# Performance work log

Hardware: AMD Instinct MI355X
Metric: run time of the kernel (lower is better)

The kernel has to match this reference:

```python
import jax, jax.numpy as jnp
import numpy as np

# dims
B, N, D, F, L = 512, 128, 256, 16, 3
EPS = 1e-7
MAX_NORM = 1.0 - 1e-5  # PoincareBall proj boundary (c = 1.0)


def _proj(x):
    """Project points into the open Poincare ball (c=1)."""
    n = jnp.maximum(jnp.linalg.norm(x, axis=-1, keepdims=True), EPS)
    scale = jnp.where(n > MAX_NORM, MAX_NORM / n, 1.0)
    return x * scale


def _expmap0(u):
    """Exponential map at the origin, c=1: tanh(||u||) * u / ||u||."""
    n = jnp.maximum(jnp.linalg.norm(u, axis=-1, keepdims=True), EPS)
    return jnp.tanh(n) * u / n


def _logmap0(x):
    """Log map at the origin, c=1: artanh(||x||) * x / ||x||."""
    n = jnp.maximum(jnp.linalg.norm(x, axis=-1, keepdims=True), EPS)
    return jnp.arctanh(jnp.minimum(n, MAX_NORM)) * x / n


def setup_inputs() -> dict:
    key = jax.random.key(0)
    ks = jax.random.split(key, 6)
    # manifold input points: small tangent vectors -> inside the ball
    x = 0.01 * jax.random.normal(ks[0], (B, N, D), dtype=jnp.float32)
    adj = jax.random.uniform(ks[1], (B, N, N), dtype=jnp.float32)
    node_mask = jnp.ones((B, N, 1), dtype=jnp.float32)
    # per-layer HGC linear weights (tangent-space linear), hidden_dim -> hidden_dim
    Ws = jax.random.normal(ks[2], (L, D, D), dtype=jnp.float32) / np.sqrt(D)
    bs = jnp.zeros((L, D), dtype=jnp.float32)
    # final masked linear: hidden_dim -> max_feat_num
    Wout = jax.random.normal(ks[3], (D, F), dtype=jnp.float32) / np.sqrt(D)
    bout = jnp.zeros((F,), dtype=jnp.float32)
    return {"x": x, "adj": adj, "node_mask": node_mask,
            "Ws": Ws, "bs": bs, "Wout": Wout, "bout": bout}


def reference(x, adj, node_mask, Ws, bs, Wout, bout):
    # HGCN decoder: stack of hyperbolic graph-conv layers on the Poincare ball
    # (logmap0 -> tangent linear -> adjacency aggregation -> ReLU -> expmap0),
    # then logmap0 and a masked linear head.
    h = _proj(x)
    for i in range(L):
        t = _logmap0(h)                                  # [B,N,D] tangent at origin
        t = t @ Ws[i] + bs[i]                            # tangent linear
        t = jnp.einsum('bij,bjd->bid', adj, t)           # sum aggregation, norm factor 1
        t = jax.nn.relu(t)                               # activation in tangent space
        h = _proj(_expmap0(t))                           # back to the manifold
    out_tan = _logmap0(h)                                # manifold.logmap0 decode
    type_pred = (out_tan @ Wout + bout) * node_mask      # [B,N,F]
    return type_pred
```

## Files before the change

kernel.cpp:

```cpp
#include <hip/hip_runtime.h>
#include <hip/hip_bf16.h>
#include <math.h>


typedef _Float16 f16;
typedef f16 f16x8 __attribute__((ext_vector_type(8)));
typedef f16 f16x4 __attribute__((ext_vector_type(4)));
typedef float f32x4 __attribute__((ext_vector_type(4)));

#define NB 512
#define NN 128
#define ND 256
#define NF 16
#define NL 3

#define EPSV   1e-7f
#define MAXN   0.99999f
#define ATHMAX 6.1030340f

__device__ __forceinline__ int sT_idx(int m, int k) {
    return m * ND + ((((k >> 3) ^ (m & 7)) << 3) | (k & 7));
}
__device__ __forceinline__ int sV_idx(int n, int j) {
    return n * NN + ((((j >> 3) ^ (n & 15)) << 3) | (j & 7));
}

__global__ void prep_kernel(const float* __restrict__ Ws,
                            const float* __restrict__ Wout,
                            f16* __restrict__ Wt, f16* __restrict__ WoutT) {
    int idx = blockIdx.x * 256 + threadIdx.x;
    if (idx < NL * ND * ND) {
        int l = idx / (ND * ND);
        int r = idx % (ND * ND);
        int n = r >> 8;
        int k = r & 255;
        Wt[idx] = (f16)Ws[l * ND * ND + k * ND + n];
    }
    if (idx < NF * ND) {
        int f = idx >> 8;
        int k = idx & 255;
        WoutT[idx] = (f16)Wout[k * NF + f];
    }
}

__global__ __launch_bounds__(1024, 4)
void hgcn_kernel(const float* __restrict__ x,
                 const float* __restrict__ adj,
                 const float* __restrict__ node_mask,
                 const f16*  __restrict__ Wt,
                 const float* __restrict__ bs,
                 const f16*  __restrict__ WoutT,
                 const float* __restrict__ bout,
                 float* __restrict__ out) {
    __shared__ __align__(16) f16 sT[NN * ND];
    __shared__ __align__(16) f16 sV[ND * NN];
    __shared__ float sRed[16 * 16];

    const int b    = blockIdx.x;
    const int tid  = threadIdx.x;
    const int wave = tid >> 6;
    const int lane = tid & 63;
    const int lg   = lane >> 4;
    const int lc   = lane & 15;

    const f32x4 fzero = {0.f, 0.f, 0.f, 0.f};

    {
        const float4* xb = (const float4*)(x + (size_t)b * NN * ND);
        #pragma unroll
        for (int r = 0; r < 8; ++r) {
            int row = wave * 8 + r;
            float4 v = xb[row * 64 + lane];
            float ssq = v.x * v.x + v.y * v.y + v.z * v.z + v.w * v.w;
            #pragma unroll
            for (int d = 1; d < 64; d <<= 1) ssq += __shfl_xor(ssq, d);
            float norm = sqrtf(ssq);
            float n1  = fmaxf(norm, EPSV);
            float sc1 = (n1 > MAXN) ? (MAXN / n1) : 1.0f;
            float hn  = norm * sc1;
            float n2  = fmaxf(hn, EPSV);
            float aa  = fminf(n2, MAXN);
            float s   = sc1 * (atanhf(aa) / n2);
            f16x4 t4;
            t4[0] = (f16)(v.x * s); t4[1] = (f16)(v.y * s);
            t4[2] = (f16)(v.z * s); t4[3] = (f16)(v.w * s);
            *(f16x4*)&sT[sT_idx(row, lane * 4)] = t4;
        }
    }

    f16x8 adjf[4];
    {
        const float* adjb = adj + (size_t)b * NN * NN;
        #pragma unroll
        for (int ks = 0; ks < 4; ++ks) {
            const float4* ap = (const float4*)(adjb + ((wave >> 1) * 16 + lc) * NN + ks * 32 + lg * 8);
            float4 alo = ap[0], ahi = ap[1];
            f16x8 a;
            a[0] = (f16)alo.x; a[1] = (f16)alo.y; a[2] = (f16)alo.z; a[3] = (f16)alo.w;
            a[4] = (f16)ahi.x; a[5] = (f16)ahi.y; a[6] = (f16)ahi.z; a[7] = (f16)ahi.w;
            adjf[ks] = a;
        }
    }
    __syncthreads();

    for (int layer = 0; layer < NL; ++layer) {
        const f16* WtL  = Wt + layer * ND * ND;
        const float bias = bs[layer * ND + wave * 16 + lc];

        f32x4 acc_a[8];
        #pragma unroll
        for (int t = 0; t < 8; ++t) acc_a[t] = fzero;

        #pragma unroll
        for (int ks = 0; ks < 8; ++ks) {
            f16x8 bfr = *(const f16x8*)(WtL + (wave * 16 + lc) * ND + ks * 32 + lg * 8);
            #pragma unroll
            for (int mt = 0; mt < 8; ++mt) {
                f16x8 afr = *(const f16x8*)&sT[sT_idx(mt * 16 + lc, ks * 32 + lg * 8)];
                acc_a[mt] = __builtin_amdgcn_mfma_f32_16x16x32_f16(afr, bfr, acc_a[mt], 0, 0, 0);
            }
        }
        #pragma unroll
        for (int mt = 0; mt < 8; ++mt) {
            f16x4 v;
            #pragma unroll
            for (int r = 0; r < 4; ++r) v[r] = (f16)(acc_a[mt][r] + bias);
            *(f16x4*)&sV[sV_idx(wave * 16 + lc, mt * 16 + lg * 4)] = v;
        }
        __syncthreads();

        f32x4 acc_b[8];
        #pragma unroll
        for (int t = 0; t < 8; ++t) acc_b[t] = fzero;

        #pragma unroll
        for (int ks = 0; ks < 4; ++ks) {
            #pragma unroll
            for (int nt = 0; nt < 8; ++nt) {
                f16x8 afr = *(const f16x8*)&sV[sV_idx(((wave & 1) * 8 + nt) * 16 + lc, ks * 32 + lg * 8)];
                acc_b[nt] = __builtin_amdgcn_mfma_f32_16x16x32_f16(afr, adjf[ks], acc_b[nt], 0, 0, 0);
            }
        }

        float ssq = 0.f;
        #pragma unroll
        for (int t = 0; t < 8; ++t)
            #pragma unroll
            for (int r = 0; r < 4; ++r) {
                float v = fmaxf(acc_b[t][r], 0.0f);
                acc_b[t][r] = v;
                ssq += v * v;
            }
        ssq += __shfl_xor(ssq, 16);
        ssq += __shfl_xor(ssq, 32);
        if (lg == 0) sRed[wave * 16 + lc] = ssq;
        __syncthreads();
        float tot = ssq + sRed[(wave ^ 1) * 16 + lc];
        float nu = sqrtf(tot);
        float scale = (nu > ATHMAX) ? (ATHMAX / nu) : 1.0f;

        #pragma unroll
        for (int nt = 0; nt < 8; ++nt) {
            f16x4 v;
            #pragma unroll
            for (int r = 0; r < 4; ++r) v[r] = (f16)(acc_b[nt][r] * scale);
            *(f16x4*)&sT[sT_idx((wave >> 1) * 16 + lc, ((wave & 1) * 8 + nt) * 16 + lg * 4)] = v;
        }
        __syncthreads();
    }

    if (wave < 8) {
        f32x4 acc = fzero;
        #pragma unroll
        for (int ks = 0; ks < 8; ++ks) {
            f16x8 afr = *(const f16x8*)&sT[sT_idx(wave * 16 + lc, ks * 32 + lg * 8)];
            f16x8 bfr = *(const f16x8*)(WoutT + lc * ND + ks * 32 + lg * 8);
            acc = __builtin_amdgcn_mfma_f32_16x16x32_f16(afr, bfr, acc, 0, 0, 0);
        }
        #pragma unroll
        for (int r = 0; r < 4; ++r) {
            int row = wave * 16 + lg * 4 + r;
            float mask = node_mask[b * NN + row];
            out[((size_t)b * NN + row) * NF + lc] = (acc[r] + bout[lc]) * mask;
        }
    }
}

extern "C" void kernel_launch(void* const* d_in, const int* in_sizes, int n_in,
                              void* d_out, int out_size, void* d_ws, size_t ws_size,
                              hipStream_t stream) {
    const float* x    = (const float*)d_in[0];
    const float* adj  = (const float*)d_in[1];
    const float* mask = (const float*)d_in[2];
    const float* Ws   = (const float*)d_in[3];
    const float* bsp  = (const float*)d_in[4];
    const float* Wout = (const float*)d_in[5];
    const float* bout = (const float*)d_in[6];

    f16* Wt    = (f16*)d_ws;
    f16* WoutT = Wt + NL * ND * ND;

    prep_kernel<<<768, 256, 0, stream>>>(Ws, Wout, Wt, WoutT);
    hgcn_kernel<<<NB, 1024, 0, stream>>>(x, adj, mask, Wt, bsp, WoutT, bout,
                                         (float*)d_out);
}
```

Before: 88.23 us.

## Retile both per-layer GEMMs into 2D wave blocks with padded LDS and prefetched weights

Each wave's work in the tangent-linear GEMM changes from a 16-column strip over all rows to a 32x64 block, and in the adjacency GEMM to a 32x64 block. Each loaded fragment now feeds more MFMAs, so there are fewer LDS reads per MFMA. The XOR-swizzled LDS layouts are replaced by padded row strides to avoid bank conflicts, and weight fragments are double-buffered from global memory. Conversions now use packed round-toward-zero f16 converts and a fast-log atanh, which slightly changes numerics and adds register pressure under the 1024-thread launch bound.

```diff
diff --git a/kernel.cpp b/kernel.cpp
--- a/kernel.cpp
+++ b/kernel.cpp
@@ -6,6 +6,8 @@
 typedef _Float16 f16;
 typedef f16 f16x8 __attribute__((ext_vector_type(8)));
 typedef f16 f16x4 __attribute__((ext_vector_type(4)));
+typedef f16 f16x2 __attribute__((ext_vector_type(2)));
+typedef __fp16 fp16x2_cv __attribute__((ext_vector_type(2)));
 typedef float f32x4 __attribute__((ext_vector_type(4)));
 
 #define NB 512
@@ -14,15 +16,20 @@
 #define NF 16
 #define NL 3
 
+#define SDT 264
+#define SDV 136
+
 #define EPSV   1e-7f
 #define MAXN   0.99999f
 #define ATHMAX 6.1030340f
 
-__device__ __forceinline__ int sT_idx(int m, int k) {
-    return m * ND + ((((k >> 3) ^ (m & 7)) << 3) | (k & 7));
-}
-__device__ __forceinline__ int sV_idx(int n, int j) {
-    return n * NN + ((((j >> 3) ^ (n & 15)) << 3) | (j & 7));
+__device__ __forceinline__ f16x4 pack4(float a, float b, float c, float d) {
+    fp16x2_cv lo = __builtin_amdgcn_cvt_pkrtz(a, b);
+    fp16x2_cv hi = __builtin_amdgcn_cvt_pkrtz(c, d);
+    f16x2 lo2, hi2;
+    __builtin_memcpy(&lo2, &lo, sizeof(lo2));
+    __builtin_memcpy(&hi2, &hi, sizeof(hi2));
+    return __builtin_shufflevector(lo2, hi2, 0, 1, 2, 3);
 }
 
 __global__ void prep_kernel(const float* __restrict__ Ws,
@@ -52,9 +59,9 @@
                  const f16*  __restrict__ WoutT,
                  const float* __restrict__ bout,
                  float* __restrict__ out) {
-    __shared__ __align__(16) f16 sT[NN * ND];
-    __shared__ __align__(16) f16 sV[ND * NN];
-    __shared__ float sRed[16 * 16];
+    __shared__ __align__(16) f16 sT[NN * SDT];
+    __shared__ __align__(16) f16 sV[ND * SDV];
+    __shared__ __align__(16) float sRed[NN * 4];
 
     const int b    = blockIdx.x;
     const int tid  = threadIdx.x;
@@ -63,7 +70,27 @@
     const int lg   = lane >> 4;
     const int lc   = lane & 15;
 
+    const int ga_mb = wave & 3;
+    const int ga_nb = wave >> 2;
+    const int gb_ip = wave >> 2;
+    const int gb_nq = wave & 3;
+
     const f32x4 fzero = {0.f, 0.f, 0.f, 0.f};
+
+    f16x8 adjf[2][4];
+    {
+        const float* adjb = adj + (size_t)b * NN * NN;
+        #pragma unroll
+        for (int it = 0; it < 2; ++it)
+            #pragma unroll
+            for (int ks = 0; ks < 4; ++ks) {
+                const float4* ap = (const float4*)(adjb + (gb_ip * 32 + it * 16 + lc) * NN + ks * 32 + lg * 8);
+                float4 alo = ap[0], ahi = ap[1];
+                f16x4 l4 = pack4(alo.x, alo.y, alo.z, alo.w);
+                f16x4 h4 = pack4(ahi.x, ahi.y, ahi.z, ahi.w);
+                adjf[it][ks] = __builtin_shufflevector(l4, h4, 0, 1, 2, 3, 4, 5, 6, 7);
+            }
+    }
 
     {
         const float4* xb = (const float4*)(x + (size_t)b * NN * ND);
@@ -75,97 +102,123 @@
             #pragma unroll
             for (int d = 1; d < 64; d <<= 1) ssq += __shfl_xor(ssq, d);
             float norm = sqrtf(ssq);
-            float n1  = fmaxf(norm, EPSV);
-            float sc1 = (n1 > MAXN) ? (MAXN / n1) : 1.0f;
-            float hn  = norm * sc1;
-            float n2  = fmaxf(hn, EPSV);
-            float aa  = fminf(n2, MAXN);
-            float s   = sc1 * (atanhf(aa) / n2);
-            f16x4 t4;
-            t4[0] = (f16)(v.x * s); t4[1] = (f16)(v.y * s);
-            t4[2] = (f16)(v.z * s); t4[3] = (f16)(v.w * s);
-            *(f16x4*)&sT[sT_idx(row, lane * 4)] = t4;
-        }
-    }
-
-    f16x8 adjf[4];
-    {
-        const float* adjb = adj + (size_t)b * NN * NN;
+            float sc1 = (norm > MAXN) ? (MAXN / norm) : 1.0f;
+            float hn  = fmaxf(norm * sc1, EPSV);
+            float aa  = fminf(hn, MAXN);
+            float ath = 0.5f * __logf((1.0f + aa) / (1.0f - aa));
+            float s   = sc1 * ath / hn;
+            *(f16x4*)&sT[row * SDT + lane * 4] =
+                pack4(v.x * s, v.y * s, v.z * s, v.w * s);
+        }
+    }
+    __syncthreads();
+
+    for (int layer = 0; layer < NL; ++layer) {
+        const f16* WtL = Wt + layer * ND * ND;
+
+        float bias[4];
+        #pragma unroll
+        for (int nt = 0; nt < 4; ++nt)
+            bias[nt] = bs[layer * ND + (ga_nb * 4 + nt) * 16 + lc];
+
+        f32x4 acc_a[2][4];
+        #pragma unroll
+        for (int mt = 0; mt < 2; ++mt)
+            #pragma unroll
+            for (int nt = 0; nt < 4; ++nt) acc_a[mt][nt] = fzero;
+
+        f16x8 bcur[4], bnxt[4];
+        #pragma unroll
+        for (int nt = 0; nt < 4; ++nt)
+            bcur[nt] = *(const f16x8*)(WtL + ((ga_nb * 4 + nt) * 16 + lc) * ND + lg * 8);
+
+        #pragma unroll
+        for (int ks = 0; ks < 8; ++ks) {
+            if (ks < 7) {
+                #pragma unroll
+                for (int nt = 0; nt < 4; ++nt)
+                    bnxt[nt] = *(const f16x8*)(WtL + ((ga_nb * 4 + nt) * 16 + lc) * ND + (ks + 1) * 32 + lg * 8);
+            }
+            f16x8 a0 = *(const f16x8*)&sT[(ga_mb * 32 +      lc) * SDT + ks * 32 + lg * 8];
+            f16x8 a1 = *(const f16x8*)&sT[(ga_mb * 32 + 16 + lc) * SDT + ks * 32 + lg * 8];
+            #pragma unroll
+            for (int nt = 0; nt < 4; ++nt) {
+                acc_a[0][nt] = __builtin_amdgcn_mfma_f32_16x16x32_f16(a0, bcur[nt], acc_a[0][nt], 0, 0, 0);
+                acc_a[1][nt] = __builtin_amdgcn_mfma_f32_16x16x32_f16(a1, bcur[nt], acc_a[1][nt], 0, 0, 0);
+            }
+            if (ks < 7) {
+                #pragma unroll
+                for (int nt = 0; nt < 4; ++nt) bcur[nt] = bnxt[nt];
+            }
+        }
+        #pragma unroll
+        for (int mt = 0; mt < 2; ++mt)
+            #pragma unroll
+            for (int nt = 0; nt < 4; ++nt) {
+                int n  = (ga_nb * 4 + nt) * 16 + lc;
+                int m0 = ga_mb * 32 + mt * 16 + lg * 4;
+                *(f16x4*)&sV[n * SDV + m0] =
+                    pack4(acc_a[mt][nt][0] + bias[nt], acc_a[mt][nt][1] + bias[nt],
+                          acc_a[mt][nt][2] + bias[nt], acc_a[mt][nt][3] + bias[nt]);
+            }
+        __syncthreads();
+
+        f32x4 acc_b[2][4];
+        #pragma unroll
+        for (int it = 0; it < 2; ++it)
+            #pragma unroll
+            for (int nt = 0; nt < 4; ++nt) acc_b[it][nt] = fzero;
+
         #pragma unroll
         for (int ks = 0; ks < 4; ++ks) {
-            const float4* ap = (const float4*)(adjb + ((wave >> 1) * 16 + lc) * NN + ks * 32 + lg * 8);
-            float4 alo = ap[0], ahi = ap[1];
-            f16x8 a;
-            a[0] = (f16)alo.x; a[1] = (f16)alo.y; a[2] = (f16)alo.z; a[3] = (f16)alo.w;
-            a[4] = (f16)ahi.x; a[5] = (f16)ahi.y; a[6] = (f16)ahi.z; a[7] = (f16)ahi.w;
-            adjf[ks] = a;
-        }
-    }
-    __syncthreads();
-
-    for (int layer = 0; layer < NL; ++layer) {
-        const f16* WtL  = Wt + layer * ND * ND;
-        const float bias = bs[layer * ND + wave * 16 + lc];
-
-        f32x4 acc_a[8];
-        #pragma unroll
-        for (int t = 0; t < 8; ++t) acc_a[t] = fzero;
-
-        #pragma unroll
-        for (int ks = 0; ks < 8; ++ks) {
-            f16x8 bfr = *(const f16x8*)(WtL + (wave * 16 + lc) * ND + ks * 32 + lg * 8);
-            #pragma unroll
-            for (int mt = 0; mt < 8; ++mt) {
-                f16x8 afr = *(const f16x8*)&sT[sT_idx(mt * 16 + lc, ks * 32 + lg * 8)];
-                acc_a[mt] = __builtin_amdgcn_mfma_f32_16x16x32_f16(afr, bfr, acc_a[mt], 0, 0, 0);
-            }
-        }
-        #pragma unroll
-        for (int mt = 0; mt < 8; ++mt) {
-            f16x4 v;
-            #pragma unroll
-            for (int r = 0; r < 4; ++r) v[r] = (f16)(acc_a[mt][r] + bias);
-            *(f16x4*)&sV[sV_idx(wave * 16 + lc, mt * 16 + lg * 4)] = v;
+            #pragma unroll
+            for (int nt = 0; nt < 4; ++nt) {
+                f16x8 afr = *(const f16x8*)&sV[((gb_nq * 4 + nt) * 16 + lc) * SDV + ks * 32 + lg * 8];
+                acc_b[0][nt] = __builtin_amdgcn_mfma_f32_16x16x32_f16(afr, adjf[0][ks], acc_b[0][nt], 0, 0, 0);
+                acc_b[1][nt] = __builtin_amdgcn_mfma_f32_16x16x32_f16(afr, adjf[1][ks], acc_b[1][nt], 0, 0, 0);
+            }
+        }
+
+        float ssq[2] = {0.f, 0.f};
+        #pragma unroll
+        for (int it = 0; it < 2; ++it)
+            #pragma unroll
+            for (int nt = 0; nt < 4; ++nt)
+                #pragma unroll
+                for (int r = 0; r < 4; ++r) {
+                    float v = fmaxf(acc_b[it][nt][r], 0.0f);
+                    acc_b[it][nt][r] = v;
+                    ssq[it] += v * v;
+                }
+        #pragma unroll
+        for (int it = 0; it < 2; ++it) {
+            ssq[it] += __shfl_xor(ssq[it], 16);
+            ssq[it] += __shfl_xor(ssq[it], 32);
+        }
+        if (lg == 0) {
+            sRed[(gb_ip * 32 +      lc) * 4 + gb_nq] = ssq[0];
+            sRed[(gb_ip * 32 + 16 + lc) * 4 + gb_nq] = ssq[1];
         }
         __syncthreads();
 
-        f32x4 acc_b[8];
-        #pragma unroll
-        for (int t = 0; t < 8; ++t) acc_b[t] = fzero;
-
-        #pragma unroll
-        for (int ks = 0; ks < 4; ++ks) {
-            #pragma unroll
-            for (int nt = 0; nt < 8; ++nt) {
-                f16x8 afr = *(const f16x8*)&sV[sV_idx(((wave & 1) * 8 + nt) * 16 + lc, ks * 32 + lg * 8)];
-                acc_b[nt] = __builtin_amdgcn_mfma_f32_16x16x32_f16(afr, adjf[ks], acc_b[nt], 0, 0, 0);
-            }
-        }
-
-        float ssq = 0.f;
-        #pragma unroll
-        for (int t = 0; t < 8; ++t)
-            #pragma unroll
-            for (int r = 0; r < 4; ++r) {
-                float v = fmaxf(acc_b[t][r], 0.0f);
-                acc_b[t][r] = v;
-                ssq += v * v;
-            }
-        ssq += __shfl_xor(ssq, 16);
-        ssq += __shfl_xor(ssq, 32);
-        if (lg == 0) sRed[wave * 16 + lc] = ssq;
-        __syncthreads();
-        float tot = ssq + sRed[(wave ^ 1) * 16 + lc];
-        float nu = sqrtf(tot);
-        float scale = (nu > ATHMAX) ? (ATHMAX / nu) : 1.0f;
-
-        #pragma unroll
-        for (int nt = 0; nt < 8; ++nt) {
-            f16x4 v;
-            #pragma unroll
-            for (int r = 0; r < 4; ++r) v[r] = (f16)(acc_b[nt][r] * scale);
-            *(f16x4*)&sT[sT_idx((wave >> 1) * 16 + lc, ((wave & 1) * 8 + nt) * 16 + lg * 4)] = v;
-        }
+        float scale[2];
+        #pragma unroll
+        for (int it = 0; it < 2; ++it) {
+            f32x4 p = *(const f32x4*)&sRed[(gb_ip * 32 + it * 16 + lc) * 4];
+            float tot = p[0] + p[1] + p[2] + p[3];
+            float nu = sqrtf(tot);
+            scale[it] = (nu > ATHMAX) ? (ATHMAX / nu) : 1.0f;
+        }
+        #pragma unroll
+        for (int it = 0; it < 2; ++it)
+            #pragma unroll
+            for (int nt = 0; nt < 4; ++nt) {
+                int i  = gb_ip * 32 + it * 16 + lc;
+                int k0 = (gb_nq * 4 + nt) * 16 + lg * 4;
+                *(f16x4*)&sT[i * SDT + k0] =
+                    pack4(acc_b[it][nt][0] * scale[it], acc_b[it][nt][1] * scale[it],
+                          acc_b[it][nt][2] * scale[it], acc_b[it][nt][3] * scale[it]);
+            }
         __syncthreads();
     }
 
@@ -173,7 +226,7 @@
         f32x4 acc = fzero;
         #pragma unroll
         for (int ks = 0; ks < 8; ++ks) {
-            f16x8 afr = *(const f16x8*)&sT[sT_idx(wave * 16 + lc, ks * 32 + lg * 8)];
+            f16x8 afr = *(const f16x8*)&sT[(wave * 16 + lc) * SDT + ks * 32 + lg * 8];
             f16x8 bfr = *(const f16x8*)(WoutT + lc * ND + ks * 32 + lg * 8);
             acc = __builtin_amdgcn_mfma_f32_16x16x32_f16(afr, bfr, acc, 0, 0, 0);
         }
```

New measurement: 147.3 us. 1.67x slower.
